# Performance work log

Hardware: AMD Instinct MI355X
Metric: run time of the kernel (lower is better)

Reference implementation:

```python
import jax, jax.numpy as jnp
import numpy as np

CARD = [3049, 10, 7, 3]
EMB = 16
HID = 64
COV = 10
B = 4096
S = 512
IN_DIM = 1 + COV + len(CARD) * EMB + 1  # 76


def setup_inputs() -> dict:
    key = jax.random.key(0)
    ks = jax.random.split(key, 12)
    target = jax.random.uniform(ks[0], (B, S), dtype=jnp.float32) * 100.0
    covariates = jax.random.normal(ks[1], (B, S, COV), dtype=jnp.float32)
    static_cats = jax.random.randint(ks[2], (B, len(CARD)), 0, 3)
    scale = jax.random.uniform(ks[3], (B, 1), dtype=jnp.float32) * 10.0 + 0.1
    emb0 = jax.random.normal(ks[4], (CARD[0], EMB), dtype=jnp.float32) * 0.1
    emb1 = jax.random.normal(ks[5], (CARD[1], EMB), dtype=jnp.float32) * 0.1
    emb2 = jax.random.normal(ks[6], (CARD[2], EMB), dtype=jnp.float32) * 0.1
    emb3 = jax.random.normal(ks[7], (CARD[3], EMB), dtype=jnp.float32) * 0.1
    w_ih = jax.random.normal(ks[8], (IN_DIM, 4 * HID), dtype=jnp.float32) / np.sqrt(IN_DIM)
    w_hh = jax.random.normal(ks[9], (HID, 4 * HID), dtype=jnp.float32) / np.sqrt(HID)
    bias = jnp.zeros((4 * HID,), dtype=jnp.float32)
    w_out = jax.random.normal(ks[10], (HID, 2), dtype=jnp.float32) / np.sqrt(HID)
    b_out = jnp.zeros((2,), dtype=jnp.float32)
    return dict(target=target, covariates=covariates, static_cats=static_cats,
                scale=scale, emb0=emb0, emb1=emb1, emb2=emb2, emb3=emb3,
                w_ih=w_ih, w_hh=w_hh, bias=bias, w_out=w_out, b_out=b_out)


def reference(target, covariates, static_cats, scale,
              emb0, emb1, emb2, emb3, w_ih, w_hh, bias, w_out, b_out):
    # static embedding concat: [B, 4*EMB]
    static_emb = jnp.concatenate([emb0[static_cats[:, 0]], emb1[static_cats[:, 1]],
                                  emb2[static_cats[:, 2]], emb3[static_cats[:, 3]]], axis=-1)
    log_scale = jnp.log1p(scale)                              # [B, 1]
    static_x = jnp.concatenate([static_emb, log_scale], -1)  # [B, 4*EMB+1]
    # teacher-forced previous scaled target: shifted target/scale, zero at t=0
    ps = target / jnp.maximum(scale, 1e-4)                    # [B, S]
    prev = jnp.concatenate([jnp.zeros_like(ps[:, :1]), ps[:, :-1]], axis=1)

    h0 = jnp.zeros((target.shape[0], w_hh.shape[0]), dtype=target.dtype)

    def step(carry, xs):
        h, c = carry
        p_t, cov_t = xs  # [B], [B, COV]
        x = jnp.concatenate([p_t[:, None], cov_t, static_x], axis=-1)  # [B, IN_DIM]
        gates = x @ w_ih + h @ w_hh + bias
        i, f, g, o = jnp.split(gates, 4, axis=-1)
        i = jax.nn.sigmoid(i)
        f = jax.nn.sigmoid(f)
        g = jnp.tanh(g)
        o = jax.nn.sigmoid(o)
        c = f * c + i * g
        h = o * jnp.tanh(c)
        raw = h @ w_out + b_out                    # [B, 2]
        mu_s = jax.nn.softplus(raw[:, 0]) + 1e-4   # [B]
        al = jax.nn.softplus(raw[:, 1]) + 1e-4     # [B]
        return (h, c), (mu_s, al)

    xs = (prev.T, jnp.swapaxes(covariates, 0, 1))  # time-major
    _, (mu_s, al) = jax.lax.scan(step, (h0, h0), xs)
    mus = mu_s.T * scale   # [B, S]
    alphas = al.T          # [B, S]
    return mus, alphas
```

## Files before the change

### kernel.cpp

```cpp
#include <hip/hip_runtime.h>

#define BB 4096
#define SS 512
#define NG 256
#define BT 16
#define NT 512
#define CH 32
#define HSTR 68
#define PSTR 16
#define SBSTR 264
#define OSTR 33

typedef __bf16 bf16_t;
typedef bf16_t bf16x8 __attribute__((ext_vector_type(8)));
typedef float  f32x4  __attribute__((ext_vector_type(4)));

__device__ __forceinline__ unsigned short f2bf(float x) {
    union { float f; unsigned u; } q{x};
    unsigned r = (q.u + 0x7fffu + ((q.u >> 16) & 1u)) >> 16;
    return (unsigned short)r;
}
__device__ __forceinline__ float bf2f(unsigned short s) {
    union { unsigned u; float f; } q{((unsigned)s) << 16};
    return q.f;
}
#define LOG2E 1.4426950408889634f
__device__ __forceinline__ float frcp_(float x)  { return __builtin_amdgcn_rcpf(x); }
__device__ __forceinline__ float fexp2_(float x) { return __builtin_amdgcn_exp2f(x); }
__device__ __forceinline__ float flog2_(float x) { return __builtin_amdgcn_logf(x); }
__device__ __forceinline__ float sigmoid_(float x) { return frcp_(1.0f + fexp2_(-LOG2E * x)); }
__device__ __forceinline__ float tanh_(float x)    { return 1.0f - 2.0f * frcp_(1.0f + fexp2_((2.0f * LOG2E) * x)); }
__device__ __forceinline__ float softplus_(float x){ return x > 20.0f ? x : 0.6931471805599453f * flog2_(1.0f + fexp2_(LOG2E * x)); }

__global__ __launch_bounds__(NT)
void deepar_kernel(const float* __restrict__ target, const float* __restrict__ cov,
                   const int* __restrict__ cats, const float* __restrict__ scale,
                   const float* __restrict__ emb0, const float* __restrict__ emb1,
                   const float* __restrict__ emb2, const float* __restrict__ emb3,
                   const float* __restrict__ w_ih, const float* __restrict__ w_hh,
                   const float* __restrict__ bias, const float* __restrict__ w_out,
                   const float* __restrict__ b_out, float* __restrict__ out)
{
    __shared__ __attribute__((aligned(16))) unsigned char smemA[2 * CH * BT * PSTR * 2];
    __shared__ __attribute__((aligned(16))) unsigned short hbuf[2][BT][HSTR];
    __shared__ float obuf[2][CH][OSTR];
    __shared__ float inv_s[BT], scl_s[BT];

    unsigned short* pcx   = (unsigned short*)smemA;
    float*          sbias = (float*)smemA;
    float*          sx    = (float*)(smemA + BT * SBSTR * 4);

    const int tid  = threadIdx.x;
    const int b0   = blockIdx.x * BT;
    const int lane = tid & 63;
    const int wv   = tid >> 6;
    const int qd   = lane >> 4;
    const int ln   = lane & 15;
    const bool is_compute = (wv < 4);
    const int tid2 = tid & 255;

    for (int i = tid; i < 2 * BT * HSTR; i += NT) ((unsigned short*)hbuf)[i] = 0;
    if (tid < BT) {
        float s = scale[b0 + tid];
        scl_s[tid] = s;
        inv_s[tid] = 1.0f / fmaxf(s, 1e-4f);
        sx[tid * 68 + 64] = log1pf(s);
    }
    if (tid < BT * 4) {
        int r = tid >> 2, e = tid & 3;
        int c = cats[(b0 + r) * 4 + e];
        const float* eb = (e == 0 ? emb0 : e == 1 ? emb1 : e == 2 ? emb2 : emb3);
        for (int j = 0; j < 16; ++j) sx[r * 68 + e * 16 + j] = eb[c * 16 + j];
    }
    __syncthreads();

    {
        const int n = tid & 255, half = tid >> 8;
        float bj = bias[n];
        float acc[8];
        #pragma unroll
        for (int r = 0; r < 8; ++r) acc[r] = bj;
        for (int k = 0; k < 65; ++k) {
            float w = w_ih[(11 + k) * NG + n];
            #pragma unroll
            for (int r = 0; r < 8; ++r) acc[r] += sx[(half * 8 + r) * 68 + k] * w;
        }
        #pragma unroll
        for (int r = 0; r < 8; ++r) sbias[(half * 8 + r) * SBSTR + n] = acc[r];
    }
    __syncthreads();

    bf16x8 bfrag[4][3];
    f32x4  sbf[4];
    if (is_compute) {
        #pragma unroll
        for (int ti = 0; ti < 4; ++ti) {
            const int n = ln + 16 * (wv + 4 * ti);
            #pragma unroll
            for (int c = 0; c < 3; ++c) {
                #pragma unroll
                for (int j = 0; j < 8; ++j) {
                    int k = qd * 8 + 32 * c + j;
                    float w;
                    if (k < 64)                  w = w_hh[k * NG + n];
                    else if (k == 64 || k == 75) w = w_ih[n];
                    else if (k <= 74)            w = w_ih[(k - 64) * NG + n];
                    else                         w = 0.0f;
                    bfrag[ti][c][j] = (bf16_t)w;
                }
            }
            #pragma unroll
            for (int r = 0; r < 4; ++r)
                sbf[ti][r] = sbias[(qd * 4 + r) * SBSTR + n];
        }
    }

    const int prow = (tid2 >> 4) & 15, po = (tid2 >> 3) & 1, pkg = tid2 & 7;
    float wo[8];
    float bo = 0.0f, pscl = 1.0f;
    int opslot = 0;
    if (!is_compute) {
        #pragma unroll
        for (int j = 0; j < 8; ++j) wo[j] = w_out[(pkg * 8 + j) * 2 + po];
        bo     = b_out[po];
        pscl   = (po == 0) ? scl_s[prow] : 1.0f;
        opslot = po * 16 + prow;
    }

    __syncthreads();

    for (int i = tid; i < (2 * CH * BT * PSTR) / 2; i += NT) ((int*)smemA)[i] = 0;
    __syncthreads();

    if (tid < 256) {
        const int row = tid >> 4, i5 = tid & 15;
        const float* cr = cov + (size_t)(b0 + row) * (SS * 10);
        #pragma unroll
        for (int j = 0; j < 20; ++j) {
            int e = i5 + 16 * j, tp = e / 10, k = e - 10 * tp;
            pcx[((0 * CH + tp) * BT + row) * PSTR + 1 + k] = f2bf(cr[e]);
        }
        float pv0 = (i5 == 0) ? 0.0f : target[(size_t)(b0 + row) * SS + i5 - 1] * inv_s[row];
        float pv1 = target[(size_t)(b0 + row) * SS + i5 + 15] * inv_s[row];
        unsigned short m0 = f2bf(pv0), m1 = f2bf(pv1);
        pcx[((0 * CH + i5) * BT + row) * PSTR + 0]       = m0;
        pcx[((0 * CH + i5) * BT + row) * PSTR + 11]      = f2bf(pv0 - bf2f(m0));
        pcx[((0 * CH + i5 + 16) * BT + row) * PSTR + 0]  = m1;
        pcx[((0 * CH + i5 + 16) * BT + row) * PSTR + 11] = f2bf(pv1 - bf2f(m1));
    }
    __syncthreads();

    bf16x8 a2 = {};
    if (is_compute && qd < 2)
        a2 = *(const bf16x8*)&pcx[((0 * CH + 0) * BT + ln) * PSTR + qd * 8];

    float cst[4] = {0.0f, 0.0f, 0.0f, 0.0f};
    float crg[20];
    #pragma unroll
    for (int j = 0; j < 20; ++j) crg[j] = 0.0f;
    float trg0 = 0.0f, trg1 = 0.0f;

    for (int t = 0; t < SS; ++t) {
        const int cur = t & 1, nxt = cur ^ 1;
        __syncthreads();

        if (is_compute) {
            const unsigned short* hb = &hbuf[cur][ln][0];
            bf16x8 a0 = *(const bf16x8*)(hb + qd * 8);
            bf16x8 a1 = *(const bf16x8*)(hb + 32 + qd * 8);

            f32x4 acc0 = __builtin_amdgcn_mfma_f32_16x16x32_bf16(a0, bfrag[0][0], sbf[0], 0, 0, 0);
            f32x4 acc1 = __builtin_amdgcn_mfma_f32_16x16x32_bf16(a0, bfrag[1][0], sbf[1], 0, 0, 0);
            f32x4 acc2 = __builtin_amdgcn_mfma_f32_16x16x32_bf16(a0, bfrag[2][0], sbf[2], 0, 0, 0);
            f32x4 acc3 = __builtin_amdgcn_mfma_f32_16x16x32_bf16(a0, bfrag[3][0], sbf[3], 0, 0, 0);
            acc0 = __builtin_amdgcn_mfma_f32_16x16x32_bf16(a1, bfrag[0][1], acc0, 0, 0, 0);
            acc1 = __builtin_amdgcn_mfma_f32_16x16x32_bf16(a1, bfrag[1][1], acc1, 0, 0, 0);
            acc2 = __builtin_amdgcn_mfma_f32_16x16x32_bf16(a1, bfrag[2][1], acc2, 0, 0, 0);
            acc3 = __builtin_amdgcn_mfma_f32_16x16x32_bf16(a1, bfrag[3][1], acc3, 0, 0, 0);
            acc0 = __builtin_amdgcn_mfma_f32_16x16x32_bf16(a2, bfrag[0][2], acc0, 0, 0, 0);
            acc1 = __builtin_amdgcn_mfma_f32_16x16x32_bf16(a2, bfrag[1][2], acc1, 0, 0, 0);
            acc2 = __builtin_amdgcn_mfma_f32_16x16x32_bf16(a2, bfrag[2][2], acc2, 0, 0, 0);
            acc3 = __builtin_amdgcn_mfma_f32_16x16x32_bf16(a2, bfrag[3][2], acc3, 0, 0, 0);

            if (t + 1 < SS && qd < 2)
                a2 = *(const bf16x8*)&pcx[((((t + 1) >> 5) & 1) * CH + ((t + 1) & 31)) * BT * PSTR
                                          + ln * PSTR + qd * 8];

            const int u = 16 * wv + ln;
            #pragma unroll
            for (int r = 0; r < 4; ++r) {
                float ig = sigmoid_(acc0[r]);
                float fg = sigmoid_(acc1[r]);
                float gg = tanh_(acc2[r]);
                float og = sigmoid_(acc3[r]);
                float cc = fg * cst[r] + ig * gg;
                cst[r] = cc;
                hbuf[nxt][qd * 4 + r][u] = f2bf(og * tanh_(cc));
            }
        } else {
            if ((t & 31) == 0 && t < 480) {
                const int row = tid2 >> 4, i5 = tid2 & 15, t0n = t + CH;
                const float* cr = cov + (size_t)(b0 + row) * (SS * 10) + t0n * 10;
                #pragma unroll
                for (int j = 0; j < 20; ++j) crg[j] = cr[i5 + 16 * j];
                const float* tr = target + (size_t)(b0 + row) * SS + t0n + i5;
                trg0 = tr[-1];
                trg1 = tr[15];
            }

            if (t > 0) {
                bf16x8 hv = *(const bf16x8*)&hbuf[cur][prow][pkg * 8];
                float p = 0.0f;
                #pragma unroll
                for (int j = 0; j < 8; ++j) p += (float)hv[j] * wo[j];
                p += __shfl_xor(p, 1);
                p += __shfl_xor(p, 2);
                p += __shfl_xor(p, 4);
                if (pkg == 0) {
                    float sp = softplus_(p + bo) + 1e-4f;
                    obuf[((t - 1) >> 5) & 1][(t - 1) & 31][opslot] = sp * pscl;
                }
            }

            if ((t & 31) == 16) {
                const int c = t >> 5;
                if (c < 15) {
                    const int row = tid2 >> 4, i5 = tid2 & 15, nb = (c + 1) & 1;
                    float pv0 = trg0 * inv_s[row];
                    float pv1 = trg1 * inv_s[row];
                    unsigned short m0 = f2bf(pv0), m1 = f2bf(pv1);
                    pcx[((nb * CH + i5) * BT + row) * PSTR + 0]       = m0;
                    pcx[((nb * CH + i5) * BT + row) * PSTR + 11]      = f2bf(pv0 - bf2f(m0));
                    pcx[((nb * CH + i5 + 16) * BT + row) * PSTR + 0]  = m1;
                    pcx[((nb * CH + i5 + 16) * BT + row) * PSTR + 11] = f2bf(pv1 - bf2f(m1));
                    #pragma unroll
                    for (int j = 0; j < 20; ++j) {
                        int e = i5 + 16 * j, tp = e / 10, k = e - 10 * tp;
                        pcx[((nb * CH + tp) * BT + row) * PSTR + 1 + k] = f2bf(crg[j]);
                    }
                }
                if (c >= 1) {
                    const int pb = (c - 1) & 1, t0p = (c - 1) << 5;
                    #pragma unroll
                    for (int h = 0; h < 4; ++h) {
                        int e = tid2 + 256 * h;
                        int tte = e & 31, rowe = (e >> 5) & 15, pe = e >> 9;
                        out[(pe ? (BB * SS) : 0) + (size_t)(b0 + rowe) * SS + t0p + tte] =
                            obuf[pb][tte][pe * 16 + rowe];
                    }
                }
            }
        }
    }

    __syncthreads();
    if (!is_compute) {
        bf16x8 hv = *(const bf16x8*)&hbuf[0][prow][pkg * 8];
        float p = 0.0f;
        #pragma unroll
        for (int j = 0; j < 8; ++j) p += (float)hv[j] * wo[j];
        p += __shfl_xor(p, 1);
        p += __shfl_xor(p, 2);
        p += __shfl_xor(p, 4);
        if (pkg == 0) {
            float sp = softplus_(p + bo) + 1e-4f;
            obuf[1][31][opslot] = sp * pscl;
        }
    }
    __syncthreads();
    #pragma unroll
    for (int h = 0; h < 2; ++h) {
        int e = tid + NT * h;
        int tte = e & 31, rowe = (e >> 5) & 15, pe = e >> 9;
        out[(pe ? (BB * SS) : 0) + (size_t)(b0 + rowe) * SS + 480 + tte] =
            obuf[1][tte][pe * 16 + rowe];
    }
}

extern "C" void kernel_launch(void* const* d_in, const int* in_sizes, int n_in,
                              void* d_out, int out_size, void* d_ws, size_t ws_size,
                              hipStream_t stream) {
    deepar_kernel<<<BB / BT, NT, 0, stream>>>(
        (const float*)d_in[0], (const float*)d_in[1], (const int*)d_in[2],
        (const float*)d_in[3], (const float*)d_in[4], (const float*)d_in[5],
        (const float*)d_in[6], (const float*)d_in[7], (const float*)d_in[8],
        (const float*)d_in[9], (const float*)d_in[10], (const float*)d_in[11],
        (const float*)d_in[12], (float*)d_out);
}
```

Baseline: 500.2 us.

## Spread LSTM gate GEMM across 16 waves with shared-memory gate exchange

The block grows from 512 to 1024 threads. Every wave now computes one 16-column gate tile with three MFMAs, and the input-projection MFMA for the next step is issued early. Gate pre-activations are exchanged through a new shared buffer so each wave applies the cell update to one row. The output head moves from shuffle-based dot products to an MFMA on wave 0. The aim is to shorten the serial per-step critical path, at the cost of a second barrier per timestep and extra shared-memory traffic.

```diff
diff --git a/kernel.cpp b/kernel.cpp
--- a/kernel.cpp
+++ b/kernel.cpp
@@ -4,11 +4,12 @@
 #define SS 512
 #define NG 256
 #define BT 16
-#define NT 512
+#define NT 1024
 #define CH 32
 #define HSTR 68
 #define PSTR 16
 #define SBSTR 264
+#define GSTR 68
 #define OSTR 33
 
 typedef __bf16 bf16_t;
@@ -43,6 +44,7 @@
 {
     __shared__ __attribute__((aligned(16))) unsigned char smemA[2 * CH * BT * PSTR * 2];
     __shared__ __attribute__((aligned(16))) unsigned short hbuf[2][BT][HSTR];
+    __shared__ float gexch[4 * BT * GSTR];
     __shared__ float obuf[2][CH][OSTR];
     __shared__ float inv_s[BT], scl_s[BT];
 
@@ -56,8 +58,8 @@
     const int wv   = tid >> 6;
     const int qd   = lane >> 4;
     const int ln   = lane & 15;
-    const bool is_compute = (wv < 4);
-    const int tid2 = tid & 255;
+    const int g    = wv >> 2;
+    const int uu   = wv & 3;
 
     for (int i = tid; i < 2 * BT * HSTR; i += NT) ((unsigned short*)hbuf)[i] = 0;
     if (tid < BT) {
@@ -75,56 +77,55 @@
     __syncthreads();
 
     {
-        const int n = tid & 255, half = tid >> 8;
+        const int n = tid & 255, q = tid >> 8;
         float bj = bias[n];
-        float acc[8];
-        #pragma unroll
-        for (int r = 0; r < 8; ++r) acc[r] = bj;
+        float acc[4];
+        #pragma unroll
+        for (int r = 0; r < 4; ++r) acc[r] = bj;
         for (int k = 0; k < 65; ++k) {
             float w = w_ih[(11 + k) * NG + n];
             #pragma unroll
-            for (int r = 0; r < 8; ++r) acc[r] += sx[(half * 8 + r) * 68 + k] * w;
-        }
-        #pragma unroll
-        for (int r = 0; r < 8; ++r) sbias[(half * 8 + r) * SBSTR + n] = acc[r];
-    }
-    __syncthreads();
-
-    bf16x8 bfrag[4][3];
-    f32x4  sbf[4];
-    if (is_compute) {
-        #pragma unroll
-        for (int ti = 0; ti < 4; ++ti) {
-            const int n = ln + 16 * (wv + 4 * ti);
-            #pragma unroll
-            for (int c = 0; c < 3; ++c) {
-                #pragma unroll
-                for (int j = 0; j < 8; ++j) {
-                    int k = qd * 8 + 32 * c + j;
-                    float w;
-                    if (k < 64)                  w = w_hh[k * NG + n];
-                    else if (k == 64 || k == 75) w = w_ih[n];
-                    else if (k <= 74)            w = w_ih[(k - 64) * NG + n];
-                    else                         w = 0.0f;
-                    bfrag[ti][c][j] = (bf16_t)w;
-                }
-            }
-            #pragma unroll
-            for (int r = 0; r < 4; ++r)
-                sbf[ti][r] = sbias[(qd * 4 + r) * SBSTR + n];
-        }
-    }
-
-    const int prow = (tid2 >> 4) & 15, po = (tid2 >> 3) & 1, pkg = tid2 & 7;
-    float wo[8];
-    float bo = 0.0f, pscl = 1.0f;
-    int opslot = 0;
-    if (!is_compute) {
-        #pragma unroll
-        for (int j = 0; j < 8; ++j) wo[j] = w_out[(pkg * 8 + j) * 2 + po];
-        bo     = b_out[po];
-        pscl   = (po == 0) ? scl_s[prow] : 1.0f;
-        opslot = po * 16 + prow;
+            for (int r = 0; r < 4; ++r) acc[r] += sx[(q * 4 + r) * 68 + k] * w;
+        }
+        #pragma unroll
+        for (int r = 0; r < 4; ++r) sbias[(q * 4 + r) * SBSTR + n] = acc[r];
+    }
+    __syncthreads();
+
+    bf16x8 bfrag[3];
+    f32x4  sbf;
+    {
+        const int n = g * 64 + uu * 16 + ln;
+        #pragma unroll
+        for (int c = 0; c < 3; ++c) {
+            #pragma unroll
+            for (int j = 0; j < 8; ++j) {
+                int k = qd * 8 + 32 * c + j;
+                float w;
+                if (k < 64)                  w = w_hh[k * NG + n];
+                else if (k == 64 || k == 75) w = w_ih[n];
+                else if (k <= 74)            w = w_ih[(k - 64) * NG + n];
+                else                         w = 0.0f;
+                bfrag[c][j] = (bf16_t)w;
+            }
+        }
+        #pragma unroll
+        for (int r = 0; r < 4; ++r)
+            sbf[r] = sbias[(qd * 4 + r) * SBSTR + n];
+    }
+
+    bf16x8 wob0, wob1;
+    f32x4  bC;
+    float  scl4[4];
+    #pragma unroll
+    for (int j = 0; j < 8; ++j) {
+        wob0[j] = (bf16_t)((ln < 2) ? w_out[(qd * 8 + j) * 2 + ln] : 0.0f);
+        wob1[j] = (bf16_t)((ln < 2) ? w_out[(32 + qd * 8 + j) * 2 + ln] : 0.0f);
+    }
+    #pragma unroll
+    for (int r = 0; r < 4; ++r) {
+        bC[r]   = (ln < 2) ? b_out[ln] : 0.0f;
+        scl4[r] = (ln == 0) ? scl_s[qd * 4 + r] : 1.0f;
     }
 
     __syncthreads();
@@ -151,10 +152,12 @@
     __syncthreads();
 
     bf16x8 a2 = {};
-    if (is_compute && qd < 2)
+    if (qd < 2)
         a2 = *(const bf16x8*)&pcx[((0 * CH + 0) * BT + ln) * PSTR + qd * 8];
-
-    float cst[4] = {0.0f, 0.0f, 0.0f, 0.0f};
+    f32x4 acc_pre = __builtin_amdgcn_mfma_f32_16x16x32_bf16(a2, bfrag[2], sbf, 0, 0, 0);
+
+    float cst = 0.0f;
+    f32x4 hacc = {};
     float crg[20];
     #pragma unroll
     for (int j = 0; j < 20; ++j) crg[j] = 0.0f;
@@ -164,114 +167,109 @@
         const int cur = t & 1, nxt = cur ^ 1;
         __syncthreads();
 
-        if (is_compute) {
-            const unsigned short* hb = &hbuf[cur][ln][0];
-            bf16x8 a0 = *(const bf16x8*)(hb + qd * 8);
-            bf16x8 a1 = *(const bf16x8*)(hb + 32 + qd * 8);
-
-            f32x4 acc0 = __builtin_amdgcn_mfma_f32_16x16x32_bf16(a0, bfrag[0][0], sbf[0], 0, 0, 0);
-            f32x4 acc1 = __builtin_amdgcn_mfma_f32_16x16x32_bf16(a0, bfrag[1][0], sbf[1], 0, 0, 0);
-            f32x4 acc2 = __builtin_amdgcn_mfma_f32_16x16x32_bf16(a0, bfrag[2][0], sbf[2], 0, 0, 0);
-            f32x4 acc3 = __builtin_amdgcn_mfma_f32_16x16x32_bf16(a0, bfrag[3][0], sbf[3], 0, 0, 0);
-            acc0 = __builtin_amdgcn_mfma_f32_16x16x32_bf16(a1, bfrag[0][1], acc0, 0, 0, 0);
-            acc1 = __builtin_amdgcn_mfma_f32_16x16x32_bf16(a1, bfrag[1][1], acc1, 0, 0, 0);
-            acc2 = __builtin_amdgcn_mfma_f32_16x16x32_bf16(a1, bfrag[2][1], acc2, 0, 0, 0);
-            acc3 = __builtin_amdgcn_mfma_f32_16x16x32_bf16(a1, bfrag[3][1], acc3, 0, 0, 0);
-            acc0 = __builtin_amdgcn_mfma_f32_16x16x32_bf16(a2, bfrag[0][2], acc0, 0, 0, 0);
-            acc1 = __builtin_amdgcn_mfma_f32_16x16x32_bf16(a2, bfrag[1][2], acc1, 0, 0, 0);
-            acc2 = __builtin_amdgcn_mfma_f32_16x16x32_bf16(a2, bfrag[2][2], acc2, 0, 0, 0);
-            acc3 = __builtin_amdgcn_mfma_f32_16x16x32_bf16(a2, bfrag[3][2], acc3, 0, 0, 0);
-
-            if (t + 1 < SS && qd < 2)
-                a2 = *(const bf16x8*)&pcx[((((t + 1) >> 5) & 1) * CH + ((t + 1) & 31)) * BT * PSTR
-                                          + ln * PSTR + qd * 8];
-
-            const int u = 16 * wv + ln;
+        if ((t & 31) == 0 && t < 480 && wv >= 8 && wv < 12) {
+            const int tid2 = tid - 512;
+            const int row = tid2 >> 4, i5 = tid2 & 15, t0n = t + CH;
+            const float* cr = cov + (size_t)(b0 + row) * (SS * 10) + t0n * 10;
+            #pragma unroll
+            for (int j = 0; j < 20; ++j) crg[j] = cr[i5 + 16 * j];
+            const float* tr = target + (size_t)(b0 + row) * SS + t0n + i5;
+            trg0 = tr[-1];
+            trg1 = tr[15];
+        }
+
+        const unsigned short* hb = &hbuf[cur][ln][0];
+        bf16x8 a0 = *(const bf16x8*)(hb + qd * 8);
+        bf16x8 a1 = *(const bf16x8*)(hb + 32 + qd * 8);
+
+        f32x4 acc = __builtin_amdgcn_mfma_f32_16x16x32_bf16(a0, bfrag[0], acc_pre, 0, 0, 0);
+        acc = __builtin_amdgcn_mfma_f32_16x16x32_bf16(a1, bfrag[1], acc, 0, 0, 0);
+
+        if (wv == 0 && t > 0) {
+            hacc = __builtin_amdgcn_mfma_f32_16x16x32_bf16(a0, wob0, bC, 0, 0, 0);
+            hacc = __builtin_amdgcn_mfma_f32_16x16x32_bf16(a1, wob1, hacc, 0, 0, 0);
+        }
+
+        {
+            float* gb = gexch + (g * BT + qd * 4) * GSTR + uu * 16 + ln;
+            #pragma unroll
+            for (int r = 0; r < 4; ++r) gb[r * GSTR] = acc[r];
+        }
+
+        if (t + 1 < SS && qd < 2)
+            a2 = *(const bf16x8*)&pcx[((((t + 1) >> 5) & 1) * CH + ((t + 1) & 31)) * BT * PSTR
+                                      + ln * PSTR + qd * 8];
+
+        __syncthreads();
+
+        {
+            const int row = wv & 15;
+            const float* gb = gexch + row * GSTR + lane;
+            float gi = gb[0 * BT * GSTR];
+            float gf = gb[1 * BT * GSTR];
+            float gg = gb[2 * BT * GSTR];
+            float go = gb[3 * BT * GSTR];
+            float cc = sigmoid_(gf) * cst + sigmoid_(gi) * tanh_(gg);
+            cst = cc;
+            float h = sigmoid_(go) * tanh_(cc);
+            *((unsigned short*)&hbuf[nxt][row][lane]) = f2bf(h);
+        }
+
+        acc_pre = __builtin_amdgcn_mfma_f32_16x16x32_bf16(a2, bfrag[2], sbf, 0, 0, 0);
+
+        if (wv == 0 && t > 0 && ln < 2) {
             #pragma unroll
             for (int r = 0; r < 4; ++r) {
-                float ig = sigmoid_(acc0[r]);
-                float fg = sigmoid_(acc1[r]);
-                float gg = tanh_(acc2[r]);
-                float og = sigmoid_(acc3[r]);
-                float cc = fg * cst[r] + ig * gg;
-                cst[r] = cc;
-                hbuf[nxt][qd * 4 + r][u] = f2bf(og * tanh_(cc));
-            }
-        } else {
-            if ((t & 31) == 0 && t < 480) {
-                const int row = tid2 >> 4, i5 = tid2 & 15, t0n = t + CH;
-                const float* cr = cov + (size_t)(b0 + row) * (SS * 10) + t0n * 10;
+                float sp = softplus_(hacc[r]) + 1e-4f;
+                obuf[((t - 1) >> 5) & 1][(t - 1) & 31][ln * 16 + qd * 4 + r] = sp * scl4[r];
+            }
+        }
+
+        if ((t & 31) == 16) {
+            const int c = t >> 5;
+            if (c < 15 && wv >= 8 && wv < 12) {
+                const int tid2 = tid - 512;
+                const int row = tid2 >> 4, i5 = tid2 & 15, nb = (c + 1) & 1;
+                float pv0 = trg0 * inv_s[row];
+                float pv1 = trg1 * inv_s[row];
+                unsigned short m0 = f2bf(pv0), m1 = f2bf(pv1);
+                pcx[((nb * CH + i5) * BT + row) * PSTR + 0]       = m0;
+                pcx[((nb * CH + i5) * BT + row) * PSTR + 11]      = f2bf(pv0 - bf2f(m0));
+                pcx[((nb * CH + i5 + 16) * BT + row) * PSTR + 0]  = m1;
+                pcx[((nb * CH + i5 + 16) * BT + row) * PSTR + 11] = f2bf(pv1 - bf2f(m1));
                 #pragma unroll
-                for (int j = 0; j < 20; ++j) crg[j] = cr[i5 + 16 * j];
-                const float* tr = target + (size_t)(b0 + row) * SS + t0n + i5;
-                trg0 = tr[-1];
-                trg1 = tr[15];
-            }
-
-            if (t > 0) {
-                bf16x8 hv = *(const bf16x8*)&hbuf[cur][prow][pkg * 8];
-                float p = 0.0f;
-                #pragma unroll
-                for (int j = 0; j < 8; ++j) p += (float)hv[j] * wo[j];
-                p += __shfl_xor(p, 1);
-                p += __shfl_xor(p, 2);
-                p += __shfl_xor(p, 4);
-                if (pkg == 0) {
-                    float sp = softplus_(p + bo) + 1e-4f;
-                    obuf[((t - 1) >> 5) & 1][(t - 1) & 31][opslot] = sp * pscl;
+                for (int j = 0; j < 20; ++j) {
+                    int e = i5 + 16 * j, tp = e / 10, k = e - 10 * tp;
+                    pcx[((nb * CH + tp) * BT + row) * PSTR + 1 + k] = f2bf(crg[j]);
                 }
             }
-
-            if ((t & 31) == 16) {
-                const int c = t >> 5;
-                if (c < 15) {
-                    const int row = tid2 >> 4, i5 = tid2 & 15, nb = (c + 1) & 1;
-                    float pv0 = trg0 * inv_s[row];
-                    float pv1 = trg1 * inv_s[row];
-                    unsigned short m0 = f2bf(pv0), m1 = f2bf(pv1);
-                    pcx[((nb * CH + i5) * BT + row) * PSTR + 0]       = m0;
-                    pcx[((nb * CH + i5) * BT + row) * PSTR + 11]      = f2bf(pv0 - bf2f(m0));
-                    pcx[((nb * CH + i5 + 16) * BT + row) * PSTR + 0]  = m1;
-                    pcx[((nb * CH + i5 + 16) * BT + row) * PSTR + 11] = f2bf(pv1 - bf2f(m1));
-                    #pragma unroll
-                    for (int j = 0; j < 20; ++j) {
-                        int e = i5 + 16 * j, tp = e / 10, k = e - 10 * tp;
-                        pcx[((nb * CH + tp) * BT + row) * PSTR + 1 + k] = f2bf(crg[j]);
-                    }
-                }
-                if (c >= 1) {
-                    const int pb = (c - 1) & 1, t0p = (c - 1) << 5;
-                    #pragma unroll
-                    for (int h = 0; h < 4; ++h) {
-                        int e = tid2 + 256 * h;
-                        int tte = e & 31, rowe = (e >> 5) & 15, pe = e >> 9;
-                        out[(pe ? (BB * SS) : 0) + (size_t)(b0 + rowe) * SS + t0p + tte] =
-                            obuf[pb][tte][pe * 16 + rowe];
-                    }
-                }
-            }
-        }
-    }
-
-    __syncthreads();
-    if (!is_compute) {
-        bf16x8 hv = *(const bf16x8*)&hbuf[0][prow][pkg * 8];
-        float p = 0.0f;
-        #pragma unroll
-        for (int j = 0; j < 8; ++j) p += (float)hv[j] * wo[j];
-        p += __shfl_xor(p, 1);
-        p += __shfl_xor(p, 2);
-        p += __shfl_xor(p, 4);
-        if (pkg == 0) {
-            float sp = softplus_(p + bo) + 1e-4f;
-            obuf[1][31][opslot] = sp * pscl;
-        }
-    }
-    __syncthreads();
-    #pragma unroll
-    for (int h = 0; h < 2; ++h) {
-        int e = tid + NT * h;
-        int tte = e & 31, rowe = (e >> 5) & 15, pe = e >> 9;
+            if (c >= 1) {
+                const int pb = (c - 1) & 1, t0p = (c - 1) << 5;
+                const int tte = tid & 31, rowe = (tid >> 5) & 15, pe = tid >> 9;
+                out[(pe ? (BB * SS) : 0) + (size_t)(b0 + rowe) * SS + t0p + tte] =
+                    obuf[pb][tte][pe * 16 + rowe];
+            }
+        }
+    }
+
+    __syncthreads();
+    if (wv == 0) {
+        const unsigned short* hb = &hbuf[0][ln][0];
+        bf16x8 a0 = *(const bf16x8*)(hb + qd * 8);
+        bf16x8 a1 = *(const bf16x8*)(hb + 32 + qd * 8);
+        hacc = __builtin_amdgcn_mfma_f32_16x16x32_bf16(a0, wob0, bC, 0, 0, 0);
+        hacc = __builtin_amdgcn_mfma_f32_16x16x32_bf16(a1, wob1, hacc, 0, 0, 0);
+        if (ln < 2) {
+            #pragma unroll
+            for (int r = 0; r < 4; ++r) {
+                float sp = softplus_(hacc[r]) + 1e-4f;
+                obuf[1][31][ln * 16 + qd * 4 + r] = sp * scl4[r];
+            }
+        }
+    }
+    __syncthreads();
+    {
+        const int tte = tid & 31, rowe = (tid >> 5) & 15, pe = tid >> 9;
         out[(pe ? (BB * SS) : 0) + (size_t)(b0 + rowe) * SS + 480 + tte] =
             obuf[1][tte][pe * 16 + rowe];
     }
```

Measured after the change: 932.6 us. 86.4% more time.

## Precompute input-gate MFMA off the critical path, fold gate scales into weights, MFMA output head

Applied to the files above, without the earlier changes.

Moves the input/covariate MFMA for step t+1 to the end of step t, so only the two recurrent h@W_hh MFMAs sit on the serial dependency chain each step. It also pre-scales the gate weights and biases by -log2e (or -2log2e for the tanh gate), which drops one multiply per activation. The output head h@w_out now runs as two MFMAs on a single producer wave instead of a scalar dot product with shuffles. The cost is extra registers held across iterations, and the risk of small numerical changes from folding the scales into bf16 weights.

```diff
diff --git a/kernel.cpp b/kernel.cpp
--- a/kernel.cpp
+++ b/kernel.cpp
@@ -28,8 +28,6 @@
 __device__ __forceinline__ float frcp_(float x)  { return __builtin_amdgcn_rcpf(x); }
 __device__ __forceinline__ float fexp2_(float x) { return __builtin_amdgcn_exp2f(x); }
 __device__ __forceinline__ float flog2_(float x) { return __builtin_amdgcn_logf(x); }
-__device__ __forceinline__ float sigmoid_(float x) { return frcp_(1.0f + fexp2_(-LOG2E * x)); }
-__device__ __forceinline__ float tanh_(float x)    { return 1.0f - 2.0f * frcp_(1.0f + fexp2_((2.0f * LOG2E) * x)); }
 __device__ __forceinline__ float softplus_(float x){ return x > 20.0f ? x : 0.6931471805599453f * flog2_(1.0f + fexp2_(LOG2E * x)); }
 
 __global__ __launch_bounds__(NT)
@@ -95,6 +93,7 @@
     if (is_compute) {
         #pragma unroll
         for (int ti = 0; ti < 4; ++ti) {
+            const float gsc = (ti == 2) ? (-2.0f * LOG2E) : (-LOG2E);
             const int n = ln + 16 * (wv + 4 * ti);
             #pragma unroll
             for (int c = 0; c < 3; ++c) {
@@ -106,25 +105,27 @@
                     else if (k == 64 || k == 75) w = w_ih[n];
                     else if (k <= 74)            w = w_ih[(k - 64) * NG + n];
                     else                         w = 0.0f;
-                    bfrag[ti][c][j] = (bf16_t)w;
+                    bfrag[ti][c][j] = (bf16_t)(w * gsc);
                 }
             }
             #pragma unroll
             for (int r = 0; r < 4; ++r)
-                sbf[ti][r] = sbias[(qd * 4 + r) * SBSTR + n];
-        }
-    }
-
-    const int prow = (tid2 >> 4) & 15, po = (tid2 >> 3) & 1, pkg = tid2 & 7;
-    float wo[8];
-    float bo = 0.0f, pscl = 1.0f;
-    int opslot = 0;
-    if (!is_compute) {
-        #pragma unroll
-        for (int j = 0; j < 8; ++j) wo[j] = w_out[(pkg * 8 + j) * 2 + po];
-        bo     = b_out[po];
-        pscl   = (po == 0) ? scl_s[prow] : 1.0f;
-        opslot = po * 16 + prow;
+                sbf[ti][r] = sbias[(qd * 4 + r) * SBSTR + n] * gsc;
+        }
+    }
+
+    bf16x8 wob0, wob1;
+    f32x4  bC;
+    float  scl4[4];
+    #pragma unroll
+    for (int j = 0; j < 8; ++j) {
+        wob0[j] = (bf16_t)((ln < 2) ? w_out[(qd * 8 + j) * 2 + ln] : 0.0f);
+        wob1[j] = (bf16_t)((ln < 2) ? w_out[(32 + qd * 8 + j) * 2 + ln] : 0.0f);
+    }
+    #pragma unroll
+    for (int r = 0; r < 4; ++r) {
+        bC[r]   = (ln < 2) ? b_out[ln] : 0.0f;
+        scl4[r] = (ln == 0) ? scl_s[qd * 4 + r] : 1.0f;
     }
 
     __syncthreads();
@@ -151,8 +152,14 @@
     __syncthreads();
 
     bf16x8 a2 = {};
-    if (is_compute && qd < 2)
-        a2 = *(const bf16x8*)&pcx[((0 * CH + 0) * BT + ln) * PSTR + qd * 8];
+    f32x4 acc_pre[4];
+    if (is_compute) {
+        if (qd < 2)
+            a2 = *(const bf16x8*)&pcx[((0 * CH + 0) * BT + ln) * PSTR + qd * 8];
+        #pragma unroll
+        for (int ti = 0; ti < 4; ++ti)
+            acc_pre[ti] = __builtin_amdgcn_mfma_f32_16x16x32_bf16(a2, bfrag[ti][2], sbf[ti], 0, 0, 0);
+    }
 
     float cst[4] = {0.0f, 0.0f, 0.0f, 0.0f};
     float crg[20];
@@ -169,18 +176,14 @@
             bf16x8 a0 = *(const bf16x8*)(hb + qd * 8);
             bf16x8 a1 = *(const bf16x8*)(hb + 32 + qd * 8);
 
-            f32x4 acc0 = __builtin_amdgcn_mfma_f32_16x16x32_bf16(a0, bfrag[0][0], sbf[0], 0, 0, 0);
-            f32x4 acc1 = __builtin_amdgcn_mfma_f32_16x16x32_bf16(a0, bfrag[1][0], sbf[1], 0, 0, 0);
-            f32x4 acc2 = __builtin_amdgcn_mfma_f32_16x16x32_bf16(a0, bfrag[2][0], sbf[2], 0, 0, 0);
-            f32x4 acc3 = __builtin_amdgcn_mfma_f32_16x16x32_bf16(a0, bfrag[3][0], sbf[3], 0, 0, 0);
+            f32x4 acc0 = __builtin_amdgcn_mfma_f32_16x16x32_bf16(a0, bfrag[0][0], acc_pre[0], 0, 0, 0);
+            f32x4 acc1 = __builtin_amdgcn_mfma_f32_16x16x32_bf16(a0, bfrag[1][0], acc_pre[1], 0, 0, 0);
+            f32x4 acc2 = __builtin_amdgcn_mfma_f32_16x16x32_bf16(a0, bfrag[2][0], acc_pre[2], 0, 0, 0);
+            f32x4 acc3 = __builtin_amdgcn_mfma_f32_16x16x32_bf16(a0, bfrag[3][0], acc_pre[3], 0, 0, 0);
             acc0 = __builtin_amdgcn_mfma_f32_16x16x32_bf16(a1, bfrag[0][1], acc0, 0, 0, 0);
             acc1 = __builtin_amdgcn_mfma_f32_16x16x32_bf16(a1, bfrag[1][1], acc1, 0, 0, 0);
             acc2 = __builtin_amdgcn_mfma_f32_16x16x32_bf16(a1, bfrag[2][1], acc2, 0, 0, 0);
             acc3 = __builtin_amdgcn_mfma_f32_16x16x32_bf16(a1, bfrag[3][1], acc3, 0, 0, 0);
-            acc0 = __builtin_amdgcn_mfma_f32_16x16x32_bf16(a2, bfrag[0][2], acc0, 0, 0, 0);
-            acc1 = __builtin_amdgcn_mfma_f32_16x16x32_bf16(a2, bfrag[1][2], acc1, 0, 0, 0);
-            acc2 = __builtin_amdgcn_mfma_f32_16x16x32_bf16(a2, bfrag[2][2], acc2, 0, 0, 0);
-            acc3 = __builtin_amdgcn_mfma_f32_16x16x32_bf16(a2, bfrag[3][2], acc3, 0, 0, 0);
 
             if (t + 1 < SS && qd < 2)
                 a2 = *(const bf16x8*)&pcx[((((t + 1) >> 5) & 1) * CH + ((t + 1) & 31)) * BT * PSTR
@@ -189,13 +192,20 @@
             const int u = 16 * wv + ln;
             #pragma unroll
             for (int r = 0; r < 4; ++r) {
-                float ig = sigmoid_(acc0[r]);
-                float fg = sigmoid_(acc1[r]);
-                float gg = tanh_(acc2[r]);
-                float og = sigmoid_(acc3[r]);
-                float cc = fg * cst[r] + ig * gg;
+                float si = frcp_(1.0f + fexp2_(acc0[r]));
+                float sf = frcp_(1.0f + fexp2_(acc1[r]));
+                float tg = 2.0f * frcp_(1.0f + fexp2_(acc2[r])) - 1.0f;
+                float so = frcp_(1.0f + fexp2_(acc3[r]));
+                float cc = sf * cst[r] + si * tg;
                 cst[r] = cc;
-                hbuf[nxt][qd * 4 + r][u] = f2bf(og * tanh_(cc));
+                float th = 2.0f * frcp_(1.0f + fexp2_((-2.0f * LOG2E) * cc)) - 1.0f;
+                *(bf16_t*)&hbuf[nxt][qd * 4 + r][u] = (bf16_t)(so * th);
+            }
+
+            if (t + 1 < SS) {
+                #pragma unroll
+                for (int ti = 0; ti < 4; ++ti)
+                    acc_pre[ti] = __builtin_amdgcn_mfma_f32_16x16x32_bf16(a2, bfrag[ti][2], sbf[ti], 0, 0, 0);
             }
         } else {
             if ((t & 31) == 0 && t < 480) {
@@ -208,17 +218,18 @@
                 trg1 = tr[15];
             }
 
-            if (t > 0) {
-                bf16x8 hv = *(const bf16x8*)&hbuf[cur][prow][pkg * 8];
-                float p = 0.0f;
-                #pragma unroll
-                for (int j = 0; j < 8; ++j) p += (float)hv[j] * wo[j];
-                p += __shfl_xor(p, 1);
-                p += __shfl_xor(p, 2);
-                p += __shfl_xor(p, 4);
-                if (pkg == 0) {
-                    float sp = softplus_(p + bo) + 1e-4f;
-                    obuf[((t - 1) >> 5) & 1][(t - 1) & 31][opslot] = sp * pscl;
+            if (wv == 4 && t > 0) {
+                const unsigned short* hb = &hbuf[cur][ln][0];
+                bf16x8 a0 = *(const bf16x8*)(hb + qd * 8);
+                bf16x8 a1 = *(const bf16x8*)(hb + 32 + qd * 8);
+                f32x4 hacc = __builtin_amdgcn_mfma_f32_16x16x32_bf16(a0, wob0, bC, 0, 0, 0);
+                hacc = __builtin_amdgcn_mfma_f32_16x16x32_bf16(a1, wob1, hacc, 0, 0, 0);
+                if (ln < 2) {
+                    #pragma unroll
+                    for (int r = 0; r < 4; ++r) {
+                        float sp = softplus_(hacc[r]) + 1e-4f;
+                        obuf[((t - 1) >> 5) & 1][(t - 1) & 31][ln * 16 + qd * 4 + r] = sp * scl4[r];
+                    }
                 }
             }
 
@@ -254,17 +265,18 @@
     }
 
     __syncthreads();
-    if (!is_compute) {
-        bf16x8 hv = *(const bf16x8*)&hbuf[0][prow][pkg * 8];
-        float p = 0.0f;
-        #pragma unroll
-        for (int j = 0; j < 8; ++j) p += (float)hv[j] * wo[j];
-        p += __shfl_xor(p, 1);
-        p += __shfl_xor(p, 2);
-        p += __shfl_xor(p, 4);
-        if (pkg == 0) {
-            float sp = softplus_(p + bo) + 1e-4f;
-            obuf[1][31][opslot] = sp * pscl;
+    if (wv == 4) {
+        const unsigned short* hb = &hbuf[0][ln][0];
+        bf16x8 a0 = *(const bf16x8*)(hb + qd * 8);
+        bf16x8 a1 = *(const bf16x8*)(hb + 32 + qd * 8);
+        f32x4 hacc = __builtin_amdgcn_mfma_f32_16x16x32_bf16(a0, wob0, bC, 0, 0, 0);
+        hacc = __builtin_amdgcn_mfma_f32_16x16x32_bf16(a1, wob1, hacc, 0, 0, 0);
+        if (ln < 2) {
+            #pragma unroll
+            for (int r = 0; r < 4; ++r) {
+                float sp = softplus_(hacc[r]) + 1e-4f;
+                obuf[1][31][ln * 16 + qd * 4 + r] = sp * scl4[r];
+            }
         }
     }
     __syncthreads();
```

Result: no change. 494.1 us (-1.2%).
